# Kernel optimization log

Measured on AMD Instinct MI355X. Metric: run time of the kernel, lower is better.

## Reference

```python
import jax, jax.numpy as jnp
import numpy as np

# Module constants (match init_kwargs)
E = 8           # num_experts
K = 2           # num_experts_per_tok
BLOCK = 16      # BLOCK_SIZE hardcoded in module
NORM_TOPK = True


def setup_inputs() -> dict:
    key = jax.random.key(0)
    k0, k1, k2, k3 = jax.random.split(key, 4)
    B, S, H = 2, 2048, 768
    F = 4 * H  # ffn_hidden_size
    x = jax.random.normal(k0, (B, S, H), dtype=jnp.float32)
    router_w = jax.random.normal(k1, (E, H), dtype=jnp.float32) * 0.02
    # kaiming-uniform-ish scale for w1/w2
    w1 = jax.random.uniform(k2, (H, E * F), dtype=jnp.float32, minval=-1.0, maxval=1.0) * float(1.0 / np.sqrt(H))
    w2 = jax.random.uniform(k3, (E * F, H), dtype=jnp.float32, minval=-1.0, maxval=1.0) * float(1.0 / np.sqrt(E * F))
    return {"x": x, "router_w": router_w, "w1": w1, "w2": w2}


def _moe_forward(x, router_w, w1, w2):
    B, S, H = x.shape
    T = B * S
    x_flat = x.reshape(T, H)

    # Router
    router_logits = x_flat @ router_w.T                      # [T, E]
    rw = jax.nn.softmax(router_logits.astype(jnp.float32), axis=-1)
    top_w, sel = jax.lax.top_k(rw, K)                        # [T, K]
    if NORM_TOPK:
        top_w = top_w / top_w.sum(axis=-1, keepdims=True)
    top_w = top_w.astype(x.dtype)  # NOTE: computed but NOT applied in combine (faithful to source)

    # Block-padding multiplicities (faithful to source's duplicate-last-token padding bug):
    # assignments are sorted stably by expert; the LAST assignment of each expert's
    # group is duplicated pad_e = (-count_e) % BLOCK times and then scatter-added.
    sel_flat = sel.reshape(-1)                               # [T*K], token-major stable order
    flat_idx = jnp.arange(T * K, dtype=jnp.int32)
    counts = jax.ops.segment_sum(jnp.ones((T * K,), jnp.int32), sel_flat, num_segments=E)
    pad = (-counts) % BLOCK                                  # [E]
    last_idx = jax.ops.segment_max(flat_idx, sel_flat, num_segments=E)  # [E]
    mult = 1 + jnp.where(flat_idx == last_idx[sel_flat], pad[sel_flat], 0)  # [T*K]

    # Combine coefficients coef[t, e] = multiplicity of (token t, expert e) assignment
    token_ids = flat_idx // K
    coef = jnp.zeros((T, E), dtype=x.dtype).at[token_ids, sel_flat].add(mult.astype(x.dtype))

    # Expert FFNs: y1 = gelu(x @ W1_e) @ W2_e, combined with coef (NOT routing weights)
    F = w1.shape[1] // E
    w1e = w1.reshape(H, E, F)
    w2e = w2.reshape(E, F, H)
    out = jnp.zeros((T, H), dtype=x.dtype)
    for e in range(E):  # small fixed loop over experts
        h = jax.nn.gelu(x_flat @ w1e[:, e, :], approximate=False)  # [T, F]
        out = out + coef[:, e:e + 1] * (h @ w2e[e])                # [T, H]

    return out.reshape(B, S, H), router_logits


def reference(x, router_w, w1, w2):
    return _moe_forward(x, router_w, w1, w2)
```

## Files before the change

kernel.cpp:

```cpp
#include <hip/hip_runtime.h>
#include <math.h>

#define T_TOK 4096
#define H_DIM 768
#define E_NUM 8
#define F_DIM 3072
#define EF_DIM 24576
#define BK 64
#define SEG_MAX 9216
#define MAX_TILES 72
#define TILE_SH (128 * BK)

#define OFF_CNT      0
#define OFF_LAST     8
#define OFF_NT      40
#define OFF_TOTAL   41
#define OFF_SCHED_E 48
#define OFF_SCHED_G 120

#define WS_SEL   768
#define WS_TOK   33536
#define WS_COEF  70400
#define WS_XG    107264ull
#define WS_HG    14263040ull
#define WS_WT    70886144ull

typedef __attribute__((ext_vector_type(8))) short short8;
typedef __attribute__((ext_vector_type(4))) float float4v;

__device__ __forceinline__ short f2b(float f) {
  union { float f; unsigned u; } v; v.f = f;
  unsigned r = v.u + 0x7FFFu + ((v.u >> 16) & 1u);
  return (short)(r >> 16);
}
__device__ __forceinline__ float b2f(short s) {
  union { unsigned u; float f; } v; v.u = ((unsigned)(unsigned short)s) << 16;
  return v.f;
}
__device__ __forceinline__ float gelu_fast(float v) {
  const float z = 1.5957691216f * fmaf(0.044715f * v * v, v, v);
  return v / (1.0f + __expf(-z));
}
__device__ __forceinline__ void gl_lds16(const void* g, void* l) {
  __builtin_amdgcn_global_load_lds(
      (const __attribute__((address_space(1))) void*)g,
      (__attribute__((address_space(3))) void*)l, 16, 0, 0);
}

__global__ __launch_bounds__(256) void router_k(const float* __restrict__ x,
                                                const float* __restrict__ rw,
                                                float* __restrict__ logits_out,
                                                int* __restrict__ sel) {
  __shared__ float rws[E_NUM * H_DIM];
  for (int i = threadIdx.x; i < E_NUM * H_DIM; i += 256) rws[i] = rw[i];
  __syncthreads();
  const int wid = threadIdx.x >> 6, lane = threadIdx.x & 63;
  const int t = blockIdx.x * 4 + wid;
  const float* xr = x + (size_t)t * H_DIM;
  double acc[E_NUM];
#pragma unroll
  for (int e = 0; e < E_NUM; ++e) acc[e] = 0.0;
  for (int i = 0; i < H_DIM / 64; ++i) {
    const int h = lane + 64 * i;
    const float xv = xr[h];
#pragma unroll
    for (int e = 0; e < E_NUM; ++e) acc[e] += (double)xv * (double)rws[e * H_DIM + h];
  }
#pragma unroll
  for (int e = 0; e < E_NUM; ++e)
    for (int off = 32; off; off >>= 1) acc[e] += __shfl_down(acc[e], off);
  if (lane == 0) {
    float lg[E_NUM];
#pragma unroll
    for (int e = 0; e < E_NUM; ++e) { lg[e] = (float)acc[e]; logits_out[t * E_NUM + e] = lg[e]; }
    int e0 = 0;
    for (int e = 1; e < E_NUM; ++e) if (lg[e] > lg[e0]) e0 = e;
    int e1 = -1;
    for (int e = 0; e < E_NUM; ++e) {
      if (e == e0) continue;
      if (e1 < 0 || lg[e] > lg[e1]) e1 = e;
    }
    sel[t * 2 + 0] = e0;
    sel[t * 2 + 1] = e1;
  }
}

__global__ __launch_bounds__(1024) void hist_k(const int* __restrict__ sel,
                                               int* __restrict__ meta) {
  const int e = blockIdx.x;
  const int tid = threadIdx.x, lane = tid & 63, wid = tid >> 6;
  __shared__ int wcnt[16], wlast[16];
  int c = 0, lmax = 0;
#pragma unroll
  for (int it = 0; it < 8; ++it) {
    const int a = it * 1024 + tid;
    const unsigned long long mask = __ballot(sel[a] == e);
    if (lane == 0 && mask) {
      c += (int)__popcll(mask);
      const int hi = 63 - (int)__clzll((long long)mask);
      const int cand = a + hi + 1;
      lmax = lmax > cand ? lmax : cand;
    }
  }
  if (lane == 0) { wcnt[wid] = c; wlast[wid] = lmax; }
  __syncthreads();
  if (tid == 0) {
    int C = 0, L = 0;
    for (int w = 0; w < 16; ++w) { C += wcnt[w]; L = L > wlast[w] ? L : wlast[w]; }
    meta[OFF_CNT + e] = C;
    meta[OFF_LAST + e] = L;
  }
}

__global__ __launch_bounds__(1024) void scatter_k(const int* __restrict__ sel,
                                                  int* __restrict__ meta,
                                                  int* __restrict__ tok,
                                                  float* __restrict__ coefv) {
  const int e = blockIdx.x;
  const int tid = threadIdx.x, lane = tid & 63, wid = tid >> 6;
  __shared__ int wv[16];

  int cnt[E_NUM];
#pragma unroll
  for (int i = 0; i < E_NUM; ++i) cnt[i] = meta[OFF_CNT + i];
  int seg = 0;
  for (int i = 0; i < e; ++i) seg += (cnt[i] + 127) & ~127;
  const int c = cnt[e];
  const int ru = (c + 127) & ~127;
  const int pad = (16 - (c & 15)) & 15;
  const int laste = meta[OFF_LAST + e];
  const float lastcoef = (float)(1 + pad);

  for (int p = c + tid; p < ru; p += 1024) { tok[seg + p] = -1; coefv[seg + p] = 0.0f; }
  if (e == E_NUM - 1) {
    const int total = seg + ru;
    for (int p = total + tid; p < SEG_MAX; p += 1024) { tok[p] = -1; coefv[p] = 0.0f; }
  }

  if (e == 0) {
    int nt = 0, s2 = 0;
    for (int i = 0; i < E_NUM; ++i) {
      const int rui = (cnt[i] + 127) & ~127;
      for (int m = 0; m < rui; m += 128) {
        if (nt == tid) { meta[OFF_SCHED_E + nt] = i; meta[OFF_SCHED_G + nt] = s2 + m; }
        ++nt;
      }
      s2 += rui;
    }
    if (tid >= nt && tid < MAX_TILES) { meta[OFF_SCHED_E + tid] = -1; meta[OFF_SCHED_G + tid] = 0; }
    if (tid == 0) { meta[OFF_NT] = nt; meta[OFF_TOTAL] = s2; }
  }

  int running = 0;
#pragma unroll
  for (int it = 0; it < 8; ++it) {
    const int a = it * 1024 + tid;
    const bool f = (sel[a] == e);
    const unsigned long long mask = __ballot(f);
    if (lane == 0) wv[wid] = (int)__popcll(mask);
    __syncthreads();
    int pre = 0, tot = 0;
#pragma unroll
    for (int w = 0; w < 16; ++w) { const int v = wv[w]; pre += (w < wid) ? v : 0; tot += v; }
    if (f) {
      const int rank = (int)__popcll(mask & ((1ull << lane) - 1ull));
      const int g = seg + running + pre + rank;
      tok[g] = a;
      coefv[g] = (laste == a + 1) ? lastcoef : 1.0f;
    }
    running += tot;
    __syncthreads();
  }
}

__global__ __launch_bounds__(256) void pos_k(const int* __restrict__ tok, int* __restrict__ pos) {
  const int g = blockIdx.x * 256 + threadIdx.x;
  const int a = tok[g];
  if (a >= 0) pos[a] = g;
}

__global__ __launch_bounds__(256) void gather_x_k(const float* __restrict__ x,
                                                  const int* __restrict__ tok,
                                                  short* __restrict__ xg) {
  const int u = blockIdx.x * 256 + threadIdx.x;
  const int g = u / 96;
  const int c = (u - g * 96) * 8;
  const int a = tok[g];
  short8 v = {0, 0, 0, 0, 0, 0, 0, 0};
  if (a >= 0) {
    const float* src = x + (size_t)(a >> 1) * H_DIM + c;
    float4v f0 = *(const float4v*)src;
    float4v f1 = *(const float4v*)(src + 4);
    v[0] = f2b(f0[0]); v[1] = f2b(f0[1]); v[2] = f2b(f0[2]); v[3] = f2b(f0[3]);
    v[4] = f2b(f1[0]); v[5] = f2b(f1[1]); v[6] = f2b(f1[2]); v[7] = f2b(f1[3]);
  }
  *(short8*)&xg[(size_t)g * H_DIM + c] = v;
}

__global__ __launch_bounds__(256) void conv_w1_k(const float* __restrict__ w1, short* __restrict__ w1t) {
  __shared__ float tile[64][65];
  const int n0 = blockIdx.x * 64;
  const int h0 = blockIdx.y * 64;
  const int tid = threadIdx.x;
  const int rr = tid >> 4;
  const int cc = (tid & 15) * 4;
#pragma unroll
  for (int p = 0; p < 4; ++p) {
    const int r = p * 16 + rr;
    float4v f = *(const float4v*)(w1 + (size_t)(h0 + r) * EF_DIM + n0 + cc);
    tile[r][cc] = f[0]; tile[r][cc + 1] = f[1]; tile[r][cc + 2] = f[2]; tile[r][cc + 3] = f[3];
  }
  __syncthreads();
#pragma unroll
  for (int p = 0; p < 2; ++p) {
    const int item = p * 256 + tid;
    const int nl = item >> 3;
    const int u8 = (item & 7) * 8;
    short8 v;
#pragma unroll
    for (int j = 0; j < 8; ++j) v[j] = f2b(tile[u8 + j][nl]);
    *(short8*)(w1t + (size_t)(n0 + nl) * H_DIM + h0 + u8) = v;
  }
}

__global__ __launch_bounds__(256) void conv_w2_k(const float* __restrict__ w2, short* __restrict__ w2t) {
  __shared__ float tile[64][65];
  const int k0 = blockIdx.x * 64;
  const int h0 = blockIdx.y * 64;
  const int e = k0 / F_DIM;
  const int f0 = k0 - e * F_DIM;
  const int tid = threadIdx.x;
  const int rr = tid >> 4;
  const int cc = (tid & 15) * 4;
#pragma unroll
  for (int p = 0; p < 4; ++p) {
    const int r = p * 16 + rr;
    float4v f = *(const float4v*)(w2 + (size_t)(k0 + r) * H_DIM + h0 + cc);
    tile[r][cc] = f[0]; tile[r][cc + 1] = f[1]; tile[r][cc + 2] = f[2]; tile[r][cc + 3] = f[3];
  }
  __syncthreads();
#pragma unroll
  for (int p = 0; p < 2; ++p) {
    const int item = p * 256 + tid;
    const int nl = item >> 3;
    const int u8 = (item & 7) * 8;
    short8 v;
#pragma unroll
    for (int j = 0; j < 8; ++j) v[j] = f2b(tile[u8 + j][nl]);
    *(short8*)(w2t + (size_t)(e * H_DIM + h0 + nl) * F_DIM + f0 + u8) = v;
  }
}


__global__ __launch_bounds__(256) void gemm1_k(const short* __restrict__ xg,
                                               const short* __restrict__ w1t,
                                               const int* __restrict__ meta,
                                               short* __restrict__ hg) {
  const unsigned hwL = blockIdx.x;
  const unsigned logical = (hwL & 7u) * 216u + (hwL >> 3);
  const int slot = (int)(logical / 24u);
  const int n0 = (int)(logical % 24u) * 128;
  if (slot >= meta[OFF_NT]) return;
  const int e = meta[OFF_SCHED_E + slot];
  const int gbase = meta[OFF_SCHED_G + slot];

  __shared__ short As[2 * TILE_SH];
  __shared__ short Bs[2 * TILE_SH];

  const int tid = threadIdx.x;
  const int w = tid >> 6, l = tid & 63;
  const int mw = (w & 1) * 64, nw = (w >> 1) * 64;
  const int lrow = l & 15, q = l >> 4;
  const int srow = l >> 3;
  const int schunk = (l & 7) ^ srow;

  const short* agp[4];
  const short* bgp[4];
  int loff[4];
#pragma unroll
  for (int i = 0; i < 4; ++i) {
    const int r = i * 32 + w * 8 + srow;
    agp[i] = xg + (size_t)(gbase + r) * H_DIM + schunk * 8;
    bgp[i] = w1t + (size_t)(e * F_DIM + n0 + r) * H_DIM + schunk * 8;
    loff[i] = (i * 32 + w * 8) * BK + l * 8;
  }
  const int rsw = lrow & 7;

  float4v acc[4][4] = {};

#pragma unroll
  for (int i = 0; i < 4; ++i) gl_lds16(agp[i], &As[loff[i]]);
#pragma unroll
  for (int i = 0; i < 4; ++i) gl_lds16(bgp[i], &Bs[loff[i]]);
  asm volatile("s_waitcnt vmcnt(0)" ::: "memory");
  __builtin_amdgcn_s_barrier();

  const int NT = H_DIM / BK;
  for (int t = 0; t < NT; ++t) {
    const int cb = (t & 1) * TILE_SH;
    const int nb = TILE_SH - cb;
    if (t + 1 < NT) {
      const int k0 = (t + 1) * BK;
#pragma unroll
      for (int i = 0; i < 4; ++i) gl_lds16(agp[i] + k0, &As[nb + loff[i]]);
#pragma unroll
      for (int i = 0; i < 4; ++i) gl_lds16(bgp[i] + k0, &Bs[nb + loff[i]]);
    }
#pragma unroll
    for (int s = 0; s < 2; ++s) {
      short8 a_frag[4], b_frag[4];
      const int csw = ((s * 4 + q) ^ rsw) * 8;
#pragma unroll
      for (int i = 0; i < 4; ++i) a_frag[i] = *(const short8*)&As[cb + (mw + 16 * i + lrow) * BK + csw];
#pragma unroll
      for (int j = 0; j < 4; ++j) b_frag[j] = *(const short8*)&Bs[cb + (nw + 16 * j + lrow) * BK + csw];
#pragma unroll
      for (int i = 0; i < 4; ++i)
#pragma unroll
        for (int j = 0; j < 4; ++j)
          acc[i][j] = __builtin_amdgcn_mfma_f32_16x16x32_bf16(a_frag[i], b_frag[j], acc[i][j], 0, 0, 0);
    }
    asm volatile("s_waitcnt vmcnt(0) lgkmcnt(0)" ::: "memory");
    __builtin_amdgcn_s_barrier();
  }

  short* Ep = As;
#pragma unroll
  for (int i = 0; i < 4; ++i)
#pragma unroll
    for (int j = 0; j < 4; ++j)
#pragma unroll
      for (int r = 0; r < 4; ++r) {
        const int row = mw + 16 * i + q * 4 + r;
        const int col = nw + 16 * j + lrow;
        Ep[row * 128 + (col ^ ((row & 7) << 4))] = f2b(gelu_fast(acc[i][j][r]));
      }
  __syncthreads();
#pragma unroll
  for (int p = 0; p < 8; ++p) {
    const int item = p * 256 + tid;
    const int row = item >> 4;
    const int cc8 = (item & 15) * 8;
    const short8 v = *(const short8*)&Ep[row * 128 + (cc8 ^ ((row & 7) << 4))];
    *(short8*)&hg[(size_t)(gbase + row) * F_DIM + n0 + cc8] = v;
  }
}

__global__ __launch_bounds__(256) void gemm2_k(const short* __restrict__ hg,
                                               const short* __restrict__ w2t,
                                               const int* __restrict__ meta,
                                               short* __restrict__ tmp) {
  const unsigned hwL = blockIdx.x;
  const unsigned logical = (hwL & 7u) * 54u + (hwL >> 3);
  const int slot = (int)(logical / 6u);
  const int n0 = (int)(logical % 6u) * 128;
  if (slot >= meta[OFF_NT]) return;
  const int e = meta[OFF_SCHED_E + slot];
  const int gbase = meta[OFF_SCHED_G + slot];

  __shared__ short As[2 * TILE_SH];
  __shared__ short Bs[2 * TILE_SH];

  const int tid = threadIdx.x;
  const int w = tid >> 6, l = tid & 63;
  const int mw = (w & 1) * 64, nw = (w >> 1) * 64;
  const int lrow = l & 15, q = l >> 4;
  const int srow = l >> 3;
  const int schunk = (l & 7) ^ srow;

  const short* agp[4];
  const short* bgp[4];
  int loff[4];
#pragma unroll
  for (int i = 0; i < 4; ++i) {
    const int r = i * 32 + w * 8 + srow;
    agp[i] = hg + (size_t)(gbase + r) * F_DIM + schunk * 8;
    bgp[i] = w2t + (size_t)(e * H_DIM + n0 + r) * F_DIM + schunk * 8;
    loff[i] = (i * 32 + w * 8) * BK + l * 8;
  }
  const int rsw = lrow & 7;

  float4v acc[4][4] = {};

#pragma unroll
  for (int i = 0; i < 4; ++i) gl_lds16(agp[i], &As[loff[i]]);
#pragma unroll
  for (int i = 0; i < 4; ++i) gl_lds16(bgp[i], &Bs[loff[i]]);
  asm volatile("s_waitcnt vmcnt(0)" ::: "memory");
  __builtin_amdgcn_s_barrier();

  const int NT = F_DIM / BK;
  for (int t = 0; t < NT; ++t) {
    const int cb = (t & 1) * TILE_SH;
    const int nb = TILE_SH - cb;
    if (t + 1 < NT) {
      const int k0 = (t + 1) * BK;
#pragma unroll
      for (int i = 0; i < 4; ++i) gl_lds16(agp[i] + k0, &As[nb + loff[i]]);
#pragma unroll
      for (int i = 0; i < 4; ++i) gl_lds16(bgp[i] + k0, &Bs[nb + loff[i]]);
    }
#pragma unroll
    for (int s = 0; s < 2; ++s) {
      short8 a_frag[4], b_frag[4];
      const int csw = ((s * 4 + q) ^ rsw) * 8;
#pragma unroll
      for (int i = 0; i < 4; ++i) a_frag[i] = *(const short8*)&As[cb + (mw + 16 * i + lrow) * BK + csw];
#pragma unroll
      for (int j = 0; j < 4; ++j) b_frag[j] = *(const short8*)&Bs[cb + (nw + 16 * j + lrow) * BK + csw];
#pragma unroll
      for (int i = 0; i < 4; ++i)
#pragma unroll
        for (int j = 0; j < 4; ++j)
          acc[i][j] = __builtin_amdgcn_mfma_f32_16x16x32_bf16(a_frag[i], b_frag[j], acc[i][j], 0, 0, 0);
    }
    asm volatile("s_waitcnt vmcnt(0) lgkmcnt(0)" ::: "memory");
    __builtin_amdgcn_s_barrier();
  }

  short* Ep = As;
#pragma unroll
  for (int i = 0; i < 4; ++i)
#pragma unroll
    for (int j = 0; j < 4; ++j)
#pragma unroll
      for (int r = 0; r < 4; ++r) {
        const int row = mw + 16 * i + q * 4 + r;
        const int col = nw + 16 * j + lrow;
        Ep[row * 128 + (col ^ ((row & 7) << 4))] = f2b(acc[i][j][r]);
      }
  __syncthreads();
#pragma unroll
  for (int p = 0; p < 8; ++p) {
    const int item = p * 256 + tid;
    const int row = item >> 4;
    const int cc8 = (item & 15) * 8;
    const short8 v = *(const short8*)&Ep[row * 128 + (cc8 ^ ((row & 7) << 4))];
    *(short8*)&tmp[(size_t)(gbase + row) * H_DIM + n0 + cc8] = v;
  }
}

__global__ __launch_bounds__(256) void combine_k(const short* __restrict__ tmp,
                                                 const int* __restrict__ pos,
                                                 const float* __restrict__ coefv,
                                                 float* __restrict__ out) {
  const int u = blockIdx.x * 256 + threadIdx.x;
  const int t = u / 96;
  const int c = (u - t * 96) * 8;
  const int g0 = pos[t * 2 + 0];
  const int g1 = pos[t * 2 + 1];
  const float c0 = coefv[g0];
  const float c1 = coefv[g1];
  const short8 v0 = *(const short8*)&tmp[(size_t)g0 * H_DIM + c];
  const short8 v1 = *(const short8*)&tmp[(size_t)g1 * H_DIM + c];
  float r[8];
#pragma unroll
  for (int j = 0; j < 8; ++j) r[j] = c0 * b2f(v0[j]) + c1 * b2f(v1[j]);
  float4v* dst = (float4v*)&out[(size_t)t * H_DIM + c];
  dst[0] = (float4v){r[0], r[1], r[2], r[3]};
  dst[1] = (float4v){r[4], r[5], r[6], r[7]};
}

extern "C" void kernel_launch(void* const* d_in, const int* in_sizes, int n_in,
                              void* d_out, int out_size, void* d_ws, size_t ws_size,
                              hipStream_t stream) {
  const float* x  = (const float*)d_in[0];
  const float* rw = (const float*)d_in[1];
  const float* w1 = (const float*)d_in[2];
  const float* w2 = (const float*)d_in[3];
  float* out = (float*)d_out;
  float* logits = out + (size_t)T_TOK * H_DIM;

  char* ws = (char*)d_ws;
  int*   meta  = (int*)ws;
  int*   sel   = (int*)(ws + WS_SEL);
  int*   tok   = (int*)(ws + WS_TOK);
  float* coefv = (float*)(ws + WS_COEF);
  short* xg    = (short*)(ws + WS_XG);
  short* hg    = (short*)(ws + WS_HG);
  short* wt    = (short*)(ws + WS_WT);

  conv_w1_k<<<dim3(EF_DIM / 64, H_DIM / 64), 256, 0, stream>>>(w1, wt);
  router_k<<<T_TOK / 4, 256, 0, stream>>>(x, rw, logits, sel);
  hist_k<<<E_NUM, 1024, 0, stream>>>(sel, meta);
  scatter_k<<<E_NUM, 1024, 0, stream>>>(sel, meta, tok, coefv);
  pos_k<<<SEG_MAX / 256, 256, 0, stream>>>(tok, sel);
  gather_x_k<<<(SEG_MAX * (H_DIM / 8)) / 256, 256, 0, stream>>>(x, tok, xg);
  gemm1_k<<<24 * MAX_TILES, 256, 0, stream>>>(xg, wt, meta, hg);
  conv_w2_k<<<dim3(EF_DIM / 64, H_DIM / 64), 256, 0, stream>>>(w2, wt);
  gemm2_k<<<6 * MAX_TILES, 256, 0, stream>>>(hg, wt, meta, xg);
  combine_k<<<(T_TOK * 96) / 256, 256, 0, stream>>>(xg, sel, coefv, out);
}
```

Before: 358.6 us.

## Load weight fragments directly from global memory into registers, bypassing LDS

In both expert GEMM kernels the B (weight) tile is no longer staged through shared memory. Each wave reads its MFMA B fragments straight from global memory into registers every k-step, and only the A (activation) tile stays double-buffered in LDS. This halves LDS footprint and LDS traffic, which may raise occupancy. In exchange, weight reads are unshared between the two waves that use the same columns, so L2 traffic doubles, and the loads are not prefetched ahead but waited on in the same iteration, which risks exposing global latency.

```diff
diff --git a/kernel.cpp b/kernel.cpp
--- a/kernel.cpp
+++ b/kernel.cpp
@@ -265,7 +265,6 @@
   const int gbase = meta[OFF_SCHED_G + slot];
 
   __shared__ short As[2 * TILE_SH];
-  __shared__ short Bs[2 * TILE_SH];
 
   const int tid = threadIdx.x;
   const int w = tid >> 6, l = tid & 63;
@@ -275,23 +274,20 @@
   const int schunk = (l & 7) ^ srow;
 
   const short* agp[4];
-  const short* bgp[4];
   int loff[4];
 #pragma unroll
   for (int i = 0; i < 4; ++i) {
     const int r = i * 32 + w * 8 + srow;
     agp[i] = xg + (size_t)(gbase + r) * H_DIM + schunk * 8;
-    bgp[i] = w1t + (size_t)(e * F_DIM + n0 + r) * H_DIM + schunk * 8;
     loff[i] = (i * 32 + w * 8) * BK + l * 8;
   }
   const int rsw = lrow & 7;
+  const short* bb = w1t + (size_t)(e * F_DIM + n0 + nw + lrow) * H_DIM + q * 8;
 
   float4v acc[4][4] = {};
 
 #pragma unroll
   for (int i = 0; i < 4; ++i) gl_lds16(agp[i], &As[loff[i]]);
-#pragma unroll
-  for (int i = 0; i < 4; ++i) gl_lds16(bgp[i], &Bs[loff[i]]);
   asm volatile("s_waitcnt vmcnt(0)" ::: "memory");
   __builtin_amdgcn_s_barrier();
 
@@ -299,27 +295,32 @@
   for (int t = 0; t < NT; ++t) {
     const int cb = (t & 1) * TILE_SH;
     const int nb = TILE_SH - cb;
+    const int k0 = t * BK;
     if (t + 1 < NT) {
-      const int k0 = (t + 1) * BK;
-#pragma unroll
-      for (int i = 0; i < 4; ++i) gl_lds16(agp[i] + k0, &As[nb + loff[i]]);
-#pragma unroll
-      for (int i = 0; i < 4; ++i) gl_lds16(bgp[i] + k0, &Bs[nb + loff[i]]);
-    }
+#pragma unroll
+      for (int i = 0; i < 4; ++i) gl_lds16(agp[i] + k0 + BK, &As[nb + loff[i]]);
+    }
+    short8 b_frag[2][4];
+#pragma unroll
+    for (int s = 0; s < 2; ++s)
+#pragma unroll
+      for (int j = 0; j < 4; ++j)
+        b_frag[s][j] = *(const short8*)(bb + (size_t)j * 16 * H_DIM + k0 + s * 32);
+    short8 a_frag[2][4];
 #pragma unroll
     for (int s = 0; s < 2; ++s) {
-      short8 a_frag[4], b_frag[4];
       const int csw = ((s * 4 + q) ^ rsw) * 8;
 #pragma unroll
-      for (int i = 0; i < 4; ++i) a_frag[i] = *(const short8*)&As[cb + (mw + 16 * i + lrow) * BK + csw];
-#pragma unroll
-      for (int j = 0; j < 4; ++j) b_frag[j] = *(const short8*)&Bs[cb + (nw + 16 * j + lrow) * BK + csw];
-#pragma unroll
       for (int i = 0; i < 4; ++i)
+        a_frag[s][i] = *(const short8*)&As[cb + (mw + 16 * i + lrow) * BK + csw];
+    }
+#pragma unroll
+    for (int s = 0; s < 2; ++s)
+#pragma unroll
+      for (int i = 0; i < 4; ++i)
 #pragma unroll
         for (int j = 0; j < 4; ++j)
-          acc[i][j] = __builtin_amdgcn_mfma_f32_16x16x32_bf16(a_frag[i], b_frag[j], acc[i][j], 0, 0, 0);
-    }
+          acc[i][j] = __builtin_amdgcn_mfma_f32_16x16x32_bf16(a_frag[s][i], b_frag[s][j], acc[i][j], 0, 0, 0);
     asm volatile("s_waitcnt vmcnt(0) lgkmcnt(0)" ::: "memory");
     __builtin_amdgcn_s_barrier();
   }
@@ -359,7 +360,6 @@
   const int gbase = meta[OFF_SCHED_G + slot];
 
   __shared__ short As[2 * TILE_SH];
-  __shared__ short Bs[2 * TILE_SH];
 
   const int tid = threadIdx.x;
   const int w = tid >> 6, l = tid & 63;
@@ -369,23 +369,20 @@
   const int schunk = (l & 7) ^ srow;
 
   const short* agp[4];
-  const short* bgp[4];
   int loff[4];
 #pragma unroll
   for (int i = 0; i < 4; ++i) {
     const int r = i * 32 + w * 8 + srow;
     agp[i] = hg + (size_t)(gbase + r) * F_DIM + schunk * 8;
-    bgp[i] = w2t + (size_t)(e * H_DIM + n0 + r) * F_DIM + schunk * 8;
     loff[i] = (i * 32 + w * 8) * BK + l * 8;
   }
   const int rsw = lrow & 7;
+  const short* bb = w2t + (size_t)(e * H_DIM + n0 + nw + lrow) * F_DIM + q * 8;
 
   float4v acc[4][4] = {};
 
 #pragma unroll
   for (int i = 0; i < 4; ++i) gl_lds16(agp[i], &As[loff[i]]);
-#pragma unroll
-  for (int i = 0; i < 4; ++i) gl_lds16(bgp[i], &Bs[loff[i]]);
   asm volatile("s_waitcnt vmcnt(0)" ::: "memory");
   __builtin_amdgcn_s_barrier();
 
@@ -393,27 +390,32 @@
   for (int t = 0; t < NT; ++t) {
     const int cb = (t & 1) * TILE_SH;
     const int nb = TILE_SH - cb;
+    const int k0 = t * BK;
     if (t + 1 < NT) {
-      const int k0 = (t + 1) * BK;
-#pragma unroll
-      for (int i = 0; i < 4; ++i) gl_lds16(agp[i] + k0, &As[nb + loff[i]]);
-#pragma unroll
-      for (int i = 0; i < 4; ++i) gl_lds16(bgp[i] + k0, &Bs[nb + loff[i]]);
-    }
+#pragma unroll
+      for (int i = 0; i < 4; ++i) gl_lds16(agp[i] + k0 + BK, &As[nb + loff[i]]);
+    }
+    short8 b_frag[2][4];
+#pragma unroll
+    for (int s = 0; s < 2; ++s)
+#pragma unroll
+      for (int j = 0; j < 4; ++j)
+        b_frag[s][j] = *(const short8*)(bb + (size_t)j * 16 * F_DIM + k0 + s * 32);
+    short8 a_frag[2][4];
 #pragma unroll
     for (int s = 0; s < 2; ++s) {
-      short8 a_frag[4], b_frag[4];
       const int csw = ((s * 4 + q) ^ rsw) * 8;
 #pragma unroll
-      for (int i = 0; i < 4; ++i) a_frag[i] = *(const short8*)&As[cb + (mw + 16 * i + lrow) * BK + csw];
-#pragma unroll
-      for (int j = 0; j < 4; ++j) b_frag[j] = *(const short8*)&Bs[cb + (nw + 16 * j + lrow) * BK + csw];
-#pragma unroll
       for (int i = 0; i < 4; ++i)
+        a_frag[s][i] = *(const short8*)&As[cb + (mw + 16 * i + lrow) * BK + csw];
+    }
+#pragma unroll
+    for (int s = 0; s < 2; ++s)
+#pragma unroll
+      for (int i = 0; i < 4; ++i)
 #pragma unroll
         for (int j = 0; j < 4; ++j)
-          acc[i][j] = __builtin_amdgcn_mfma_f32_16x16x32_bf16(a_frag[i], b_frag[j], acc[i][j], 0, 0, 0);
-    }
+          acc[i][j] = __builtin_amdgcn_mfma_f32_16x16x32_bf16(a_frag[s][i], b_frag[s][j], acc[i][j], 0, 0, 0);
     asm volatile("s_waitcnt vmcnt(0) lgkmcnt(0)" ::: "memory");
     __builtin_amdgcn_s_barrier();
   }
```

Result: slower. 433.3 us (+20.8%).
